# Kernel optimization log

Hardware: AMD Instinct MI355X
Metric: run time of the kernel (lower is better)

Reference implementation:

```python
import jax, jax.numpy as jnp
import numpy as np

B, C, OC, K, HW = 32, 256, 256, 3, 56
M, G = 2, 2
GAP = max(16, C // 16)          # input_gap = 16
MO = M * OC                      # fc1 out channels = 512
FC2_OUT = OC * C * K * K         # 589824
PER = FC2_OUT // MO              # per-group out channels of fc2 = 1152


def setup_inputs() -> dict:
    key = jax.random.key(0)
    ks = jax.random.split(key, 6)
    x = jax.random.normal(ks[0], (B, C, HW, HW), dtype=jnp.float32)
    reduce_w = jax.random.normal(ks[1], (GAP, C), dtype=jnp.float32) / np.sqrt(C)
    reduce_b = jnp.zeros((GAP,), dtype=jnp.float32)
    fc1_w = jax.random.normal(ks[2], (MO, GAP), dtype=jnp.float32) / np.sqrt(GAP)
    # fc2: grouped 1x1 conv, groups=G*OC=512, 1 in-channel per group -> weight (FC2_OUT,)
    fc2_w = jax.random.normal(ks[3], (FC2_OUT,), dtype=jnp.float32)
    fc2_b = jax.random.normal(ks[4], (FC2_OUT,), dtype=jnp.float32) * 0.01
    return {"x": x, "reduce_w": reduce_w, "reduce_b": reduce_b,
            "fc1_w": fc1_w, "fc2_w": fc2_w, "fc2_b": fc2_b}


def reference(x, reduce_w, reduce_b, fc1_w, fc2_w, fc2_b):
    b, c, h, w = x.shape
    # global average pool -> (b, C)
    gap = x.mean(axis=(2, 3))
    # reduce: 1x1 conv on 1x1 map == linear
    g = gap @ reduce_w.T + reduce_b                      # (b, GAP)
    # fc1 (no bias) + sigmoid
    a = jax.nn.sigmoid(g @ fc1_w.T)                      # (b, MO)
    # fc2: grouped 1x1 conv with 1 input channel per group:
    # out[:, g*PER + j] = a[:, g] * fc2_w[g*PER + j] + fc2_b[g*PER + j]
    wk = a[:, :, None] * fc2_w.reshape(MO, PER)[None] + fc2_b.reshape(MO, PER)[None]
    wk = wk.reshape(b * OC, c, K, K)                     # per-sample conv kernels
    pad = K // 2
    y = jax.lax.conv_general_dilated(
        x.reshape(1, b * c, h, w), wk,
        window_strides=(1, 1), padding=[(pad, pad), (pad, pad)],
        feature_group_count=b,
        dimension_numbers=("NCHW", "OIHW", "NCHW"))
    return y.reshape(b, OC, y.shape[2], y.shape[3])
```

## Files before the change

kernel.cpp:

```cpp
#include <hip/hip_runtime.h>
#include <hip/hip_bf16.h>
#include <stdint.h>

#define NB   32
#define NC   256
#define NOC  256
#define HWD  56
#define NPIX 3136
#define PW   58
#define PPIX 3364
#define KTOT 2304
#define MOD  512
#define GAPD 16

#define XBT_BYTES ((size_t)NB * PPIX * NC * 2)
#define WA_BYTES  ((size_t)NB * NOC * KTOT * 2)

typedef __bf16 bf16x8 __attribute__((ext_vector_type(8)));
typedef float  f32x4  __attribute__((ext_vector_type(4)));
typedef unsigned short u16x8 __attribute__((ext_vector_type(8)));

__device__ __forceinline__ unsigned short f2bf(float f) {
    union { float f; unsigned int u; } v; v.f = f;
    unsigned int u = v.u;
    return (unsigned short)((u + 0x7FFFu + ((u >> 16) & 1u)) >> 16);
}

__global__ void se_kernel(const float* __restrict__ gap,
                          const float* __restrict__ rw, const float* __restrict__ rb,
                          const float* __restrict__ f1w, float* __restrict__ a2) {
    __shared__ float sgap[NB * NC];
    __shared__ float sg[NB * GAPD];
    int t = threadIdx.x;
    #pragma unroll
    for (int i = 0; i < 16; ++i) sgap[i * 512 + t] = gap[i * 512 + t];
    __syncthreads();
    {
        int b = t >> 4, tt = t & 15;
        float s = rb[tt];
        for (int c = 0; c < NC; ++c) s += sgap[b * NC + c] * rw[tt * NC + c];
        sg[b * GAPD + tt] = s;
    }
    __syncthreads();
    for (int i = 0; i < 32; ++i) {
        int o = i * 512 + t;
        int b = o >> 9, m = o & 511;
        float s = 0.f;
        #pragma unroll
        for (int tt = 0; tt < GAPD; ++tt) s += sg[b * GAPD + tt] * f1w[m * GAPD + tt];
        a2[o] = 1.0f / (1.0f + __expf(-s));
    }
}

__global__ void wk_kernel(const float* __restrict__ a2,
                          const float* __restrict__ f2w, const float* __restrict__ f2b,
                          unsigned short* __restrict__ wa) {
    __shared__ float sw[KTOT];
    __shared__ float sbv[KTOT];
    __shared__ float sa[2 * NB];
    int oc = blockIdx.x, c = threadIdx.x;
    const float4* wsrc = (const float4*)(f2w + (size_t)oc * KTOT);
    const float4* bsrc = (const float4*)(f2b + (size_t)oc * KTOT);
    #pragma unroll
    for (int i = 0; i < 3; ++i) {
        int idx = i * 256 + c;
        if (idx < 576) {
            ((float4*)sw)[idx] = wsrc[idx];
            ((float4*)sbv)[idx] = bsrc[idx];
        }
    }
    if (c < 64) sa[c] = a2[(c >> 1) * MOD + 2 * oc + (c & 1)];
    __syncthreads();
    float w9[9], b9[9];
    #pragma unroll
    for (int s = 0; s < 9; ++s) { w9[s] = sw[c * 9 + s]; b9[s] = sbv[c * 9 + s]; }
    bool hi = (c * 9 + 8) >= 1152;
    for (int b = 0; b < NB; ++b) {
        float a0 = sa[2 * b], a1 = sa[2 * b + 1];
        unsigned short* dst = wa + (size_t)(b * NOC + oc) * KTOT;
        #pragma unroll
        for (int s = 0; s < 9; ++s) {
            float a = ((c * 9 + s) >= 1152) ? a1 : a0;
            dst[s * NC + c] = f2bf(a * w9[s] + b9[s]);
        }
    }
    (void)hi;
}

__global__ void halo_kernel(unsigned short* __restrict__ xbt) {
    int b = blockIdx.x, t = threadIdx.x;
    unsigned short* xb = xbt + (size_t)b * PPIX * NC;
    u16x8 z = {};
    for (int i = t; i < 3712; i += 256) {
        int r = (i >= 1856) ? 1 : 0;
        int c = i - r * 1856;
        int pix = r * (57 * 58) + (c >> 5);
        *(u16x8*)(xb + (size_t)pix * NC + (c & 31) * 8) = z;
    }
    for (int i = t; i < 3584; i += 256) {
        int row = 1 + (i >> 6);
        int side = (i >> 5) & 1;
        int pix = row * PW + side * 57;
        *(u16x8*)(xb + (size_t)pix * NC + (i & 31) * 8) = z;
    }
}

#define TSTR 59
__global__ void xpose_kernel(const float* __restrict__ x, unsigned short* __restrict__ xbt,
                             float* __restrict__ gap) {
    __shared__ unsigned short tile[NC * TSTR];
    int py = blockIdx.x, b = blockIdx.y, t = threadIdx.x;
    int wv = t >> 6, l = t & 63;
    const float* xs = x + (size_t)b * NC * NPIX + py * HWD;
    int q = l & 15;
    int rb4 = l >> 4;
    #pragma unroll
    for (int it = 0; it < 16; ++it) {
        int c = wv * 64 + it * 4 + rb4;
        if (q < 14) {
            float4 v = *(const float4*)(xs + (size_t)c * NPIX + q * 4);
            unsigned short* tr = tile + c * TSTR + q * 4;
            tr[0] = f2bf(v.x); tr[1] = f2bf(v.y); tr[2] = f2bf(v.z); tr[3] = f2bf(v.w);
        }
    }
    __syncthreads();
    {
        float s = 0.f;
        #pragma unroll
        for (int px = 0; px < 56; ++px) {
            union { unsigned int u; float f; } cv;
            cv.u = ((unsigned int)tile[t * TSTR + px]) << 16;
            s += cv.f;
        }
        atomicAdd(&gap[b * NC + t], s * (1.0f / NPIX));
    }
    int cch = t & 31, pg = t >> 5;
    for (int i = 0; i < 7; ++i) {
        int px = pg * 7 + i;
        u16x8 v;
        #pragma unroll
        for (int j = 0; j < 8; ++j) v[j] = tile[(cch * 8 + j) * TSTR + px];
        *(u16x8*)(xbt + ((size_t)b * PPIX + (size_t)(1 + py) * PW + 1 + px) * NC + cch * 8) = v;
    }
}

#define SLICE 26624
#define BOFF  16384
#define PXT   160

__global__ __launch_bounds__(256, 2) void conv_gemm(
    const unsigned short* __restrict__ wa,
    const unsigned short* __restrict__ xbt,
    float* __restrict__ out)
{
    __shared__ __attribute__((aligned(16))) char lds[3 * SLICE];

    const int bid = blockIdx.x;
    const int wg  = (bid & 7) * 80 + (bid >> 3);
    const int b   = wg / 20, nt = wg % 20;

    const int t = threadIdx.x;
    const int w = t >> 6, l = t & 63;
    const int wm = w >> 1, wn = w & 1;

    const unsigned short* waB = wa + (size_t)b * NOC * KTOT;
    const unsigned short* xbB = xbt + (size_t)b * PPIX * NC;

    const unsigned short* srcA[4];
    #pragma unroll
    for (int i = 0; i < 4; ++i) {
        int e = i * 4 + w;
        int s = e * 64 + l;
        int u = s >> 3, p3 = s & 7;
        int d = p3 ^ (u & 7);
        int kq = d >> 1, sub = d & 1;
        int row = 2 * u + sub;
        srcA[i] = waB + (size_t)row * KTOT + kq * 8;
    }
    const unsigned short* srcB[3];
    int actB[3];
    #pragma unroll
    for (int i = 0; i < 3; ++i) {
        int e = (i + 4) * 4 + w;
        actB[i] = (e < 26);
        int s = (e - 16) * 64 + l;
        if (s > 639) s = 639;
        int u = s >> 3, p3 = s & 7;
        int d = p3 ^ (u & 7);
        int kq = d >> 1, sub = d & 1;
        int prow = 2 * u + sub;
        int pg = nt * PXT + prow; if (pg > NPIX - 1) pg = NPIX - 1;
        int py = pg / 56, px = pg - py * 56;
        srcB[i] = xbB + (size_t)((py + 1) * PW + (px + 1)) * NC + kq * 8;
    }
    const int l16 = l * 16;

    auto issue = [&](int tp, int slot) {
        char* sb = lds + slot * SLICE;
        const int s9 = tp >> 3;
        const int dy = (s9 >= 6) ? 2 : ((s9 >= 3) ? 1 : 0);
        const int dx = s9 - dy * 3;
        const int bsh = ((dy - 1) * PW + (dx - 1)) * NC + (tp & 7) * 32;
        #pragma unroll
        for (int i = 0; i < 4; ++i) {
            int e = i * 4 + w;
            __builtin_amdgcn_global_load_lds(
                (const __attribute__((address_space(1))) void*)(srcA[i] + tp * 32),
                (__attribute__((address_space(3))) void*)(sb + e * 1024 + l16), 16, 0, 0);
        }
        #pragma unroll
        for (int i = 0; i < 3; ++i) {
            if (actB[i]) {
                int e = (i + 4) * 4 + w;
                __builtin_amdgcn_global_load_lds(
                    (const __attribute__((address_space(1))) void*)(srcB[i] + bsh),
                    (__attribute__((address_space(3))) void*)(sb + e * 1024 + l16), 16, 0, 0);
            }
        }
    };

    const int subq = ((l >> 4) << 1) | (l & 1);
    const int ulow = (l >> 1) & 7;
    const int aoff0 = (wm * 64 + ((l & 15) >> 1)) * 128 + ((subq ^ ulow) << 4);
    const int boff0 = BOFF + (wn * 40 + ((l & 15) >> 1)) * 128 + ((subq ^ ulow) << 4);

    f32x4 acc[8][5] = {};

    issue(0, 0); issue(1, 1);

    int cs = 0, is2 = 2;
    for (int p = 0; p < 71; ++p) {
        asm volatile("s_waitcnt vmcnt(6)" ::: "memory");
        __builtin_amdgcn_s_barrier();
        __builtin_amdgcn_sched_barrier(0);
        if (p < 70) {
            issue(p + 2, is2);
            ++is2; if (is2 == 3) is2 = 0;
        }
        const char* sb = lds + cs * SLICE;
        ++cs; if (cs == 3) cs = 0;
        bf16x8 af[8];
        #pragma unroll
        for (int m = 0; m < 8; ++m)
            af[m] = *(const bf16x8*)(sb + aoff0 + m * 1024);
        __builtin_amdgcn_s_setprio(1);
        #pragma unroll
        for (int j = 0; j < 5; ++j) {
            bf16x8 bf = *(const bf16x8*)(sb + boff0 + j * 1024);
            #pragma unroll
            for (int m = 0; m < 8; ++m)
                acc[m][j] = __builtin_amdgcn_mfma_f32_16x16x32_bf16(af[m], bf, acc[m][j], 0, 0, 0);
        }
        __builtin_amdgcn_s_setprio(0);
    }
    asm volatile("s_waitcnt vmcnt(0)" ::: "memory");
    __builtin_amdgcn_s_barrier();
    __builtin_amdgcn_sched_barrier(0);
    {
        const char* sb = lds + cs * SLICE;
        bf16x8 af[8];
        #pragma unroll
        for (int m = 0; m < 8; ++m)
            af[m] = *(const bf16x8*)(sb + aoff0 + m * 1024);
        #pragma unroll
        for (int j = 0; j < 5; ++j) {
            bf16x8 bf = *(const bf16x8*)(sb + boff0 + j * 1024);
            #pragma unroll
            for (int m = 0; m < 8; ++m)
                acc[m][j] = __builtin_amdgcn_mfma_f32_16x16x32_bf16(af[m], bf, acc[m][j], 0, 0, 0);
        }
    }

    const int ocb = wm * 128 + ((l >> 4) << 2);
    const int pxb = nt * PXT + wn * 80 + (l & 15);
    #pragma unroll
    for (int i = 0; i < 8; ++i) {
        #pragma unroll
        for (int j = 0; j < 5; ++j) {
            int p = pxb + j * 16;
            if (p < NPIX) {
                float* o = out + ((size_t)(b * NOC + ocb + i * 16)) * NPIX + p;
                o[0]        = acc[i][j][0];
                o[NPIX]     = acc[i][j][1];
                o[2 * NPIX] = acc[i][j][2];
                o[3 * NPIX] = acc[i][j][3];
            }
        }
    }
}

extern "C" void kernel_launch(void* const* d_in, const int* in_sizes, int n_in,
                              void* d_out, int out_size, void* d_ws, size_t ws_size,
                              hipStream_t stream) {
    (void)in_sizes; (void)n_in; (void)out_size; (void)ws_size;
    const float* x   = (const float*)d_in[0];
    const float* rw  = (const float*)d_in[1];
    const float* rb  = (const float*)d_in[2];
    const float* f1w = (const float*)d_in[3];
    const float* f2w = (const float*)d_in[4];
    const float* f2b = (const float*)d_in[5];
    float* out = (float*)d_out;

    char* wsb = (char*)d_ws;
    unsigned short* xbt = (unsigned short*)wsb;
    unsigned short* wa  = (unsigned short*)(wsb + XBT_BYTES);
    float* gap = (float*)(wsb + XBT_BYTES + WA_BYTES);
    float* a2  = (float*)(wsb + XBT_BYTES + WA_BYTES + (size_t)NB * NC * 4);

    hipMemsetAsync(gap, 0, (size_t)NB * NC * 4, stream);
    halo_kernel<<<dim3(32), 256, 0, stream>>>(xbt);
    xpose_kernel<<<dim3(56, 32), 256, 0, stream>>>(x, xbt, gap);
    se_kernel<<<dim3(1), 512, 0, stream>>>(gap, rw, rb, f1w, a2);
    wk_kernel<<<dim3(256), 256, 0, stream>>>(a2, f2w, f2b, wa);
    conv_gemm<<<dim3(640), 256, 0, stream>>>(wa, xbt, out);
}
```

Measured before the change: 219.0 us.

## Shrink conv GEMM pixel tile to 128 and simplify LDS swizzle layout

The conv GEMM pixel tile per workgroup drops from 160 to 128, so the grid grows from 640 to 800 blocks and the accumulator grid goes from 8x5 to 8x4. The A and B LDS slices use a new, simpler 16-row by 4-quad XOR swizzle with uniform per-lane source addressing, which removes the inactive-load predicate for B. The main loop now computes the current slot before issuing the next prefetch and peels two tail computations. The aim is cleaner address math, no partial B loads and fewer registers, at the cost of less reuse of A per block and a less even wave count across the CUs.

```diff
diff --git a/kernel.cpp b/kernel.cpp
--- a/kernel.cpp
+++ b/kernel.cpp
@@ -74,7 +74,6 @@
     float w9[9], b9[9];
     #pragma unroll
     for (int s = 0; s < 9; ++s) { w9[s] = sw[c * 9 + s]; b9[s] = sbv[c * 9 + s]; }
-    bool hi = (c * 9 + 8) >= 1152;
     for (int b = 0; b < NB; ++b) {
         float a0 = sa[2 * b], a1 = sa[2 * b + 1];
         unsigned short* dst = wa + (size_t)(b * NOC + oc) * KTOT;
@@ -84,7 +83,6 @@
             dst[s * NC + c] = f2bf(a * w9[s] + b9[s]);
         }
     }
-    (void)hi;
 }
 
 __global__ void halo_kernel(unsigned short* __restrict__ xbt) {
@@ -144,9 +142,8 @@
     }
 }
 
-#define SLICE 26624
-#define BOFF  16384
-#define PXT   160
+#define SLICE 24576
+#define BOFS  16384
 
 __global__ __launch_bounds__(256, 2) void conv_gemm(
     const unsigned short* __restrict__ wa,
@@ -156,8 +153,8 @@
     __shared__ __attribute__((aligned(16))) char lds[3 * SLICE];
 
     const int bid = blockIdx.x;
-    const int wg  = (bid & 7) * 80 + (bid >> 3);
-    const int b   = wg / 20, nt = wg % 20;
+    const int wg  = (bid & 7) * 100 + (bid >> 3);
+    const int b   = wg / 25, nt = wg % 25;
 
     const int t = threadIdx.x;
     const int w = t >> 6, l = t & 63;
@@ -166,117 +163,94 @@
     const unsigned short* waB = wa + (size_t)b * NOC * KTOT;
     const unsigned short* xbB = xbt + (size_t)b * PPIX * NC;
 
+    const int srow = l >> 2;
+    const int sq8  = ((l & 3) ^ ((l >> 3) & 3)) * 8;
     const unsigned short* srcA[4];
     #pragma unroll
     for (int i = 0; i < 4; ++i) {
-        int e = i * 4 + w;
-        int s = e * 64 + l;
-        int u = s >> 3, p3 = s & 7;
-        int d = p3 ^ (u & 7);
-        int kq = d >> 1, sub = d & 1;
-        int row = 2 * u + sub;
-        srcA[i] = waB + (size_t)row * KTOT + kq * 8;
-    }
-    const unsigned short* srcB[3];
-    int actB[3];
-    #pragma unroll
-    for (int i = 0; i < 3; ++i) {
-        int e = (i + 4) * 4 + w;
-        actB[i] = (e < 26);
-        int s = (e - 16) * 64 + l;
-        if (s > 639) s = 639;
-        int u = s >> 3, p3 = s & 7;
-        int d = p3 ^ (u & 7);
-        int kq = d >> 1, sub = d & 1;
-        int prow = 2 * u + sub;
-        int pg = nt * PXT + prow; if (pg > NPIX - 1) pg = NPIX - 1;
+        int row = (i * 4 + w) * 16 + srow;
+        srcA[i] = waB + (size_t)row * KTOT + sq8;
+    }
+    const unsigned short* srcB[2];
+    #pragma unroll
+    for (int i = 0; i < 2; ++i) {
+        int row = (i * 4 + w) * 16 + srow;
+        int pg = nt * 128 + row; if (pg > NPIX - 1) pg = NPIX - 1;
         int py = pg / 56, px = pg - py * 56;
-        srcB[i] = xbB + (size_t)((py + 1) * PW + (px + 1)) * NC + kq * 8;
+        srcB[i] = xbB + (size_t)((py + 1) * PW + (px + 1)) * NC + sq8;
     }
     const int l16 = l * 16;
 
     auto issue = [&](int tp, int slot) {
         char* sb = lds + slot * SLICE;
+        const int koff = tp * 32;
         const int s9 = tp >> 3;
         const int dy = (s9 >= 6) ? 2 : ((s9 >= 3) ? 1 : 0);
         const int dx = s9 - dy * 3;
         const int bsh = ((dy - 1) * PW + (dx - 1)) * NC + (tp & 7) * 32;
         #pragma unroll
-        for (int i = 0; i < 4; ++i) {
-            int e = i * 4 + w;
+        for (int i = 0; i < 4; ++i)
             __builtin_amdgcn_global_load_lds(
-                (const __attribute__((address_space(1))) void*)(srcA[i] + tp * 32),
-                (__attribute__((address_space(3))) void*)(sb + e * 1024 + l16), 16, 0, 0);
-        }
-        #pragma unroll
-        for (int i = 0; i < 3; ++i) {
-            if (actB[i]) {
-                int e = (i + 4) * 4 + w;
-                __builtin_amdgcn_global_load_lds(
-                    (const __attribute__((address_space(1))) void*)(srcB[i] + bsh),
-                    (__attribute__((address_space(3))) void*)(sb + e * 1024 + l16), 16, 0, 0);
-            }
-        }
+                (const __attribute__((address_space(1))) void*)(srcA[i] + koff),
+                (__attribute__((address_space(3))) void*)(sb + (i * 4 + w) * 1024 + l16), 16, 0, 0);
+        #pragma unroll
+        for (int i = 0; i < 2; ++i)
+            __builtin_amdgcn_global_load_lds(
+                (const __attribute__((address_space(1))) void*)(srcB[i] + bsh),
+                (__attribute__((address_space(3))) void*)(sb + BOFS + (i * 4 + w) * 1024 + l16), 16, 0, 0);
     };
 
-    const int subq = ((l >> 4) << 1) | (l & 1);
-    const int ulow = (l >> 1) & 7;
-    const int aoff0 = (wm * 64 + ((l & 15) >> 1)) * 128 + ((subq ^ ulow) << 4);
-    const int boff0 = BOFF + (wn * 40 + ((l & 15) >> 1)) * 128 + ((subq ^ ulow) << 4);
-
-    f32x4 acc[8][5] = {};
+    const int physq16 = (((l >> 4) ^ ((l >> 1) & 3)) << 4);
+    const int arow = (l & 15) << 6;
+
+    f32x4 acc[8][4] = {};
+
+    auto compute = [&](int slot) {
+        const char* sb = lds + slot * SLICE;
+        bf16x8 af[8], bfr[4];
+        #pragma unroll
+        for (int i = 0; i < 8; ++i)
+            af[i] = *(const bf16x8*)(sb + (wm * 8 + i) * 1024 + arow + physq16);
+        #pragma unroll
+        for (int j = 0; j < 4; ++j)
+            bfr[j] = *(const bf16x8*)(sb + BOFS + (wn * 4 + j) * 1024 + arow + physq16);
+        __builtin_amdgcn_s_setprio(1);
+        #pragma unroll
+        for (int i = 0; i < 8; ++i)
+            #pragma unroll
+            for (int j = 0; j < 4; ++j)
+                acc[i][j] = __builtin_amdgcn_mfma_f32_16x16x32_bf16(af[i], bfr[j], acc[i][j], 0, 0, 0);
+        __builtin_amdgcn_s_setprio(0);
+    };
 
     issue(0, 0); issue(1, 1);
 
-    int cs = 0, is2 = 2;
-    for (int p = 0; p < 71; ++p) {
+    int cs = 0;
+    for (int p = 0; p < 70; ++p) {
         asm volatile("s_waitcnt vmcnt(6)" ::: "memory");
         __builtin_amdgcn_s_barrier();
         __builtin_amdgcn_sched_barrier(0);
-        if (p < 70) {
-            issue(p + 2, is2);
-            ++is2; if (is2 == 3) is2 = 0;
-        }
-        const char* sb = lds + cs * SLICE;
+        compute(cs);
+        int ns = cs + 2; if (ns >= 3) ns -= 3;
+        issue(p + 2, ns);
         ++cs; if (cs == 3) cs = 0;
-        bf16x8 af[8];
-        #pragma unroll
-        for (int m = 0; m < 8; ++m)
-            af[m] = *(const bf16x8*)(sb + aoff0 + m * 1024);
-        __builtin_amdgcn_s_setprio(1);
-        #pragma unroll
-        for (int j = 0; j < 5; ++j) {
-            bf16x8 bf = *(const bf16x8*)(sb + boff0 + j * 1024);
-            #pragma unroll
-            for (int m = 0; m < 8; ++m)
-                acc[m][j] = __builtin_amdgcn_mfma_f32_16x16x32_bf16(af[m], bf, acc[m][j], 0, 0, 0);
-        }
-        __builtin_amdgcn_s_setprio(0);
-    }
+    }
+    asm volatile("s_waitcnt vmcnt(6)" ::: "memory");
+    __builtin_amdgcn_s_barrier();
+    __builtin_amdgcn_sched_barrier(0);
+    compute(cs);
+    ++cs; if (cs == 3) cs = 0;
     asm volatile("s_waitcnt vmcnt(0)" ::: "memory");
     __builtin_amdgcn_s_barrier();
     __builtin_amdgcn_sched_barrier(0);
-    {
-        const char* sb = lds + cs * SLICE;
-        bf16x8 af[8];
-        #pragma unroll
-        for (int m = 0; m < 8; ++m)
-            af[m] = *(const bf16x8*)(sb + aoff0 + m * 1024);
-        #pragma unroll
-        for (int j = 0; j < 5; ++j) {
-            bf16x8 bf = *(const bf16x8*)(sb + boff0 + j * 1024);
-            #pragma unroll
-            for (int m = 0; m < 8; ++m)
-                acc[m][j] = __builtin_amdgcn_mfma_f32_16x16x32_bf16(af[m], bf, acc[m][j], 0, 0, 0);
-        }
-    }
+    compute(cs);
 
     const int ocb = wm * 128 + ((l >> 4) << 2);
-    const int pxb = nt * PXT + wn * 80 + (l & 15);
+    const int pxb = nt * 128 + wn * 64 + (l & 15);
     #pragma unroll
     for (int i = 0; i < 8; ++i) {
         #pragma unroll
-        for (int j = 0; j < 5; ++j) {
+        for (int j = 0; j < 4; ++j) {
             int p = pxb + j * 16;
             if (p < NPIX) {
                 float* o = out + ((size_t)(b * NOC + ocb + i * 16)) * NPIX + p;
@@ -312,5 +286,5 @@
     xpose_kernel<<<dim3(56, 32), 256, 0, stream>>>(x, xbt, gap);
     se_kernel<<<dim3(1), 512, 0, stream>>>(gap, rw, rb, f1w, a2);
     wk_kernel<<<dim3(256), 256, 0, stream>>>(a2, f2w, f2b, wa);
-    conv_gemm<<<dim3(640), 256, 0, stream>>>(wa, xbt, out);
-}
+    conv_gemm<<<dim3(800), 256, 0, stream>>>(wa, xbt, out);
+}
```

New measurement: 210.1 us. 1.04x faster.
